# Optimization experiments

Measured on AMD Instinct MI355X. Metric: run time of the kernel, lower is better.

Reference implementation:

```python
import jax, jax.numpy as jnp
import numpy as np

N, IN, OUT, RANK = 8192, 4096, 4096, 16
SCALING = 2.0

def setup_inputs() -> dict:
    key = jax.random.key(0)
    k1, k2, k3, k4 = jax.random.split(key, 4)
    x = jax.random.normal(k1, (N, IN), dtype=jnp.float32)
    weight = jax.random.normal(k2, (OUT, IN), dtype=jnp.float32) * (1.0 / np.sqrt(IN))
    lora_A = jax.random.normal(k3, (RANK, IN), dtype=jnp.float32) * (1.0 / np.sqrt(IN))
    lora_B = jax.random.normal(k4, (OUT, RANK), dtype=jnp.float32) * 0.01
    return {"x": x, "weight": weight, "lora_A": lora_A, "lora_B": lora_B}

def reference(x, weight, lora_A, lora_B):
    # frozen base linear: F.linear(x, weight) == x @ weight.T  -> [N, OUT]
    base = jnp.einsum('ni,oi->no', x, weight)
    # LoRA branch: dropout(x) (p=0 => identity) @ A.T @ B.T, scaled
    lora = jnp.einsum('ni,ri->nr', x, lora_A)      # [N, RANK]
    lora = jnp.einsum('nr,or->no', lora, lora_B)   # [N, OUT]
    return base + lora * SCALING
```

## Files before the change

kernel.cpp:

```cpp
#include <hip/hip_runtime.h>


#define N_ROWS 8192
#define K_DIM  4096
#define N_COLS 4096
#define RANK   16
#define BK     32
#define NT     (K_DIM / BK)

#define XBLK ((N_ROWS * K_DIM / 4) / 256)
#define WBLK ((N_COLS * K_DIM / 4) / 256)

typedef __bf16 bf16x8 __attribute__((ext_vector_type(8)));
typedef float  f32x4  __attribute__((ext_vector_type(4)));

__device__ __forceinline__ unsigned short f2bf(float f) {
  unsigned int u = __builtin_bit_cast(unsigned int, f);
  u += 0x7FFFu + ((u >> 16) & 1u);
  return (unsigned short)(u >> 16);
}


__global__ __launch_bounds__(256) void prep_kernel(const float* __restrict__ x,
                                                   const float* __restrict__ w,
                                                   const float* __restrict__ A,
                                                   const float* __restrict__ Bm,
                                                   unsigned short* __restrict__ xb,
                                                   unsigned short* __restrict__ wb) {
  const int b = blockIdx.x;
  if (b < XBLK) {
    size_t idx = (size_t)b * 256 + threadIdx.x;
    const float4 v = *reinterpret_cast<const float4*>(x + idx * 4);
    ushort4 r;
    r.x = f2bf(v.x); r.y = f2bf(v.y); r.z = f2bf(v.z); r.w = f2bf(v.w);
    *reinterpret_cast<ushort4*>(xb + idx * 4) = r;
  } else {
    size_t idx = (size_t)(b - XBLK) * 256 + threadIdx.x;
    int o  = (int)(idx >> 10);
    int ic = (int)(idx & 1023) << 2;
    const float4 wv = *reinterpret_cast<const float4*>(w + (size_t)o * K_DIM + ic);
    float a0 = wv.x, a1 = wv.y, a2 = wv.z, a3 = wv.w;
    float br[RANK];
#pragma unroll
    for (int r4 = 0; r4 < RANK / 4; ++r4) {
      const float4 bv = *reinterpret_cast<const float4*>(Bm + (size_t)o * RANK + r4 * 4);
      br[r4 * 4 + 0] = bv.x; br[r4 * 4 + 1] = bv.y;
      br[r4 * 4 + 2] = bv.z; br[r4 * 4 + 3] = bv.w;
    }
#pragma unroll
    for (int r = 0; r < RANK; ++r) {
      const float4 av = *reinterpret_cast<const float4*>(A + (size_t)r * K_DIM + ic);
      float b2 = br[r] * 2.0f;
      a0 += b2 * av.x; a1 += b2 * av.y; a2 += b2 * av.z; a3 += b2 * av.w;
    }
    ushort4 rr;
    rr.x = f2bf(a0); rr.y = f2bf(a1); rr.z = f2bf(a2); rr.w = f2bf(a3);
    *reinterpret_cast<ushort4*>(wb + (size_t)o * K_DIM + ic) = rr;
  }
}


__device__ __forceinline__ void gload_lds16(const void* g, void* l) {
  __builtin_amdgcn_global_load_lds(
      (__attribute__((address_space(1))) void*)g,
      (__attribute__((address_space(3))) void*)l, 16, 0, 0);
}

__global__ __launch_bounds__(512, 1) void gemm_bf16_r10(
    const unsigned short* __restrict__ xb, const unsigned short* __restrict__ wb,
    float* __restrict__ out) {
  __shared__ __align__(16) char smem[131072];

  const int t  = threadIdx.x;
  const int l  = t & 63;
  const int wv = t >> 6;
  const int lr = l & 15;
  const int lk = l >> 4;
  const int wr = wv >> 2;
  const int wc = wv & 3;

  const int bid  = blockIdx.x;
  const int sbid = (bid & 7) * 64 + (bid >> 3);
  const int bm   = sbid >> 4;
  const int bn   = sbid & 15;

  const int slog  = (t & 7) ^ ((t >> 3) & 7);
  const int s_row = 2 * (t >> 3) + (slog >> 2);
  const int s_k   = (slog & 3) * 8;
  const unsigned short* gA = xb + (size_t)(bm * 256 + s_row) * K_DIM + s_k;
  const unsigned short* gB = wb + (size_t)(bn * 256 + s_row) * K_DIM + s_k;

#define STG_A(BUFB, KT) do {                                                    \
    const unsigned short* _g = gA + (size_t)(KT) * BK;                          \
    char* _l = smem + (BUFB) + t * 16;                                          \
    gload_lds16(_g, _l);                                                        \
    gload_lds16(_g + (size_t)128 * K_DIM, _l + 8192);                           \
  } while (0)
#define STG_B(BUFB, KT) do {                                                    \
    const unsigned short* _g = gB + (size_t)(KT) * BK;                          \
    char* _l = smem + (BUFB) + 16384 + t * 16;                                  \
    gload_lds16(_g, _l);                                                        \
    gload_lds16(_g + (size_t)128 * K_DIM, _l + 8192);                           \
  } while (0)

  const int lane_off = (lr >> 1) * 128 + (((((lr & 1) << 2) | lk) ^ (lr >> 1)) << 4);
  const int a_base = wr * 1024 + lane_off;
  const int b_base = 16384 + wc * 1024 + lane_off;

  bf16x8 sA0[8], sB0[4], sA1[8], sB1[4];
  f32x4 acc[8][4];
#pragma unroll
  for (int m = 0; m < 8; ++m)
#pragma unroll
    for (int n = 0; n < 4; ++n)
      acc[m][n] = (f32x4){0.f, 0.f, 0.f, 0.f};

#define RD_SET(SA, SB, RB) do {                                                 \
    _Pragma("unroll")                                                           \
    for (int m = 0; m < 8; ++m)                                                 \
      SA[m] = *(const bf16x8*)(smem + (RB) + a_base + m * 2048);                \
    _Pragma("unroll")                                                           \
    for (int n = 0; n < 4; ++n)                                                 \
      SB[n] = *(const bf16x8*)(smem + (RB) + b_base + n * 4096);                \
  } while (0)

#define MF_SET(SA, SB) do {                                                     \
    _Pragma("unroll")                                                           \
    for (int m = 0; m < 8; ++m)                                                 \
      _Pragma("unroll")                                                         \
      for (int n = 0; n < 4; ++n)                                               \
        acc[m][n] = __builtin_amdgcn_mfma_f32_16x16x32_bf16(                    \
            SA[m], SB[n], acc[m][n], 0, 0, 0);                                  \
  } while (0)

#define BODY(RB_OFF, SB_OFF, CUR_A, CUR_B, NXT_A, NXT_B, TT) do {               \
    const int _ts = ((TT) + 3 < NT) ? (TT) + 3 : NT - 1;                        \
    STG_A(SB_OFF, _ts); STG_B(SB_OFF, _ts);                                     \
    RD_SET(NXT_A, NXT_B, RB_OFF);                                               \
    __builtin_amdgcn_s_setprio(1);                                              \
    MF_SET(CUR_A, CUR_B);                                                       \
    __builtin_amdgcn_s_setprio(0);                                              \
    __builtin_amdgcn_sched_barrier(0);                                          \
    asm volatile("s_waitcnt vmcnt(4)");                                         \
    __builtin_amdgcn_s_barrier();                                               \
    __builtin_amdgcn_sched_barrier(0);                                          \
  } while (0)

  STG_A(0, 0);      STG_B(0, 0);
  STG_A(32768, 1);  STG_B(32768, 1);
  STG_A(65536, 2);  STG_B(65536, 2);
  __builtin_amdgcn_sched_barrier(0);
  asm volatile("s_waitcnt vmcnt(4)");
  __builtin_amdgcn_s_barrier();
  __builtin_amdgcn_sched_barrier(0);
  RD_SET(sA0, sB0, 0);

#pragma nounroll
  for (int u = 0; u < NT / 4; ++u) {
    const int tb = 4 * u;
    BODY(32768, 98304, sA0, sB0, sA1, sB1, tb);
    BODY(65536, 0,     sA1, sB1, sA0, sB0, tb + 1);
    BODY(98304, 32768, sA0, sB0, sA1, sB1, tb + 2);
    BODY(0,     65536, sA1, sB1, sA0, sB0, tb + 3);
  }

  const int orow = bm * 256 + wr * 16 + lk * 4;
  const int ocol = bn * 256 + wc * 16 + lr;
#pragma unroll
  for (int mf = 0; mf < 8; ++mf)
#pragma unroll
    for (int nf = 0; nf < 4; ++nf)
#pragma unroll
      for (int j = 0; j < 4; ++j)
        out[(size_t)(orow + mf * 32 + j) * N_COLS + (ocol + nf * 64)] = acc[mf][nf][j];

#undef STG_A
#undef STG_B
#undef RD_SET
#undef MF_SET
#undef BODY
}


__global__ __launch_bounds__(256) void fallback_kernel(const float* __restrict__ x,
                                                       const float* __restrict__ w,
                                                       const float* __restrict__ A,
                                                       const float* __restrict__ Bm,
                                                       float* __restrict__ out) {
  const int o    = blockIdx.x * 256 + threadIdx.x;
  const int nrow = blockIdx.y;
  float bro[RANK];
#pragma unroll
  for (int r = 0; r < RANK; ++r) bro[r] = Bm[(size_t)o * RANK + r] * 2.0f;
  float bacc = 0.f;
  float tacc[RANK];
#pragma unroll
  for (int r = 0; r < RANK; ++r) tacc[r] = 0.f;
  for (int k = 0; k < K_DIM; ++k) {
    float xv = x[(size_t)nrow * K_DIM + k];
    bacc += xv * w[(size_t)o * K_DIM + k];
#pragma unroll
    for (int r = 0; r < RANK; ++r) tacc[r] += xv * A[(size_t)r * K_DIM + k];
  }
  float res = bacc;
#pragma unroll
  for (int r = 0; r < RANK; ++r) res += bro[r] * tacc[r];
  out[(size_t)nrow * N_COLS + o] = res;
}


extern "C" void kernel_launch(void* const* d_in, const int* in_sizes, int n_in,
                              void* d_out, int out_size, void* d_ws, size_t ws_size,
                              hipStream_t stream) {
  const float* x  = (const float*)d_in[0];
  const float* w  = (const float*)d_in[1];
  const float* A  = (const float*)d_in[2];
  const float* Bm = (const float*)d_in[3];
  float* out = (float*)d_out;

  const size_t need = ((size_t)N_ROWS * K_DIM + (size_t)N_COLS * K_DIM) * sizeof(unsigned short);
  if (ws_size < need) {
    dim3 grid(N_COLS / 256, N_ROWS);
    fallback_kernel<<<grid, 256, 0, stream>>>(x, w, A, Bm, out);
    return;
  }

  unsigned short* xb = (unsigned short*)d_ws;
  unsigned short* wb = xb + (size_t)N_ROWS * K_DIM;

  prep_kernel<<<XBLK + WBLK, 256, 0, stream>>>(x, w, A, Bm, xb, wb);

  const int grid_gemm = (N_ROWS / 256) * (N_COLS / 256);
  gemm_bf16_r10<<<grid_gemm, 512, 0, stream>>>(xb, wb, out);
}
```

Baseline: 325.3 us.

## Shrink GEMM tile to 256x128 with double-buffered LDS for multi-block occupancy

The bf16 MFMA GEMM goes from a 256x256 tile with a 4-stage, 128KB LDS ring and a register-double-buffered fragment pipeline to a 256x128 tile with 48KB double-buffered LDS. Launch bounds now allow up to 4 blocks per CU, and the grid doubles. The aim is to hide latency through occupancy rather than deep software prefetch. In exchange, each step waits on vmcnt(0) with only one tile of lookahead, operand reuse per block is lower, and there is more global traffic for A.

```diff
diff --git a/kernel.cpp b/kernel.cpp
--- a/kernel.cpp
+++ b/kernel.cpp
@@ -5,8 +5,8 @@
 #define K_DIM  4096
 #define N_COLS 4096
 #define RANK   16
-#define BK     32
-#define NT     (K_DIM / BK)
+#define BKS    32
+#define NSTEP  (K_DIM / BKS)
 
 #define XBLK ((N_ROWS * K_DIM / 4) / 256)
 #define WBLK ((N_COLS * K_DIM / 4) / 256)
@@ -66,119 +66,109 @@
       (__attribute__((address_space(3))) void*)l, 16, 0, 0);
 }
 
-__global__ __launch_bounds__(512, 1) void gemm_bf16_r10(
+__global__ __launch_bounds__(512, 4) void gemm_bf16_r12(
     const unsigned short* __restrict__ xb, const unsigned short* __restrict__ wb,
     float* __restrict__ out) {
-  __shared__ __align__(16) char smem[131072];
+  __shared__ __align__(16) char smem[49152];
 
   const int t  = threadIdx.x;
   const int l  = t & 63;
   const int wv = t >> 6;
   const int lr = l & 15;
   const int lk = l >> 4;
-  const int wr = wv >> 2;
-  const int wc = wv & 3;
+  const int wr = wv >> 1;
+  const int wc = wv & 1;
 
   const int bid  = blockIdx.x;
-  const int sbid = (bid & 7) * 64 + (bid >> 3);
-  const int bm   = sbid >> 4;
-  const int bn   = sbid & 15;
+  const int sbid = (bid & 7) * 128 + (bid >> 3);
+  const int bm   = sbid >> 5;
+  const int bn   = sbid & 31;
 
   const int slog  = (t & 7) ^ ((t >> 3) & 7);
   const int s_row = 2 * (t >> 3) + (slog >> 2);
   const int s_k   = (slog & 3) * 8;
   const unsigned short* gA = xb + (size_t)(bm * 256 + s_row) * K_DIM + s_k;
-  const unsigned short* gB = wb + (size_t)(bn * 256 + s_row) * K_DIM + s_k;
-
-#define STG_A(BUFB, KT) do {                                                    \
-    const unsigned short* _g = gA + (size_t)(KT) * BK;                          \
-    char* _l = smem + (BUFB) + t * 16;                                          \
-    gload_lds16(_g, _l);                                                        \
-    gload_lds16(_g + (size_t)128 * K_DIM, _l + 8192);                           \
-  } while (0)
-#define STG_B(BUFB, KT) do {                                                    \
-    const unsigned short* _g = gB + (size_t)(KT) * BK;                          \
-    char* _l = smem + (BUFB) + 16384 + t * 16;                                  \
-    gload_lds16(_g, _l);                                                        \
-    gload_lds16(_g + (size_t)128 * K_DIM, _l + 8192);                           \
+  const unsigned short* gB = wb + (size_t)(bn * 128 + s_row) * K_DIM + s_k;
+  char* ldsA = smem + t * 16;
+  char* ldsB = smem + 16384 + t * 16;
+
+#define STG(BUFB, KT) do {                                                      \
+    const unsigned short* _ga = gA + (size_t)(KT) * BKS;                        \
+    const unsigned short* _gb = gB + (size_t)(KT) * BKS;                        \
+    gload_lds16(_ga, ldsA + (BUFB));                                            \
+    gload_lds16(_ga + (size_t)128 * K_DIM, ldsA + (BUFB) + 8192);               \
+    gload_lds16(_gb, ldsB + (BUFB));                                            \
   } while (0)
 
   const int lane_off = (lr >> 1) * 128 + (((((lr & 1) << 2) | lk) ^ (lr >> 1)) << 4);
-  const int a_base = wr * 1024 + lane_off;
-  const int b_base = 16384 + wc * 1024 + lane_off;
-
-  bf16x8 sA0[8], sB0[4], sA1[8], sB1[4];
-  f32x4 acc[8][4];
-#pragma unroll
-  for (int m = 0; m < 8; ++m)
+  const int a_base = wr * 4096 + lane_off;
+  const int b_base = 16384 + wc * 4096 + lane_off;
+
+  bf16x8 aF[4], bF[4];
+  f32x4 acc[4][4];
+#pragma unroll
+  for (int m = 0; m < 4; ++m)
 #pragma unroll
     for (int n = 0; n < 4; ++n)
       acc[m][n] = (f32x4){0.f, 0.f, 0.f, 0.f};
 
-#define RD_SET(SA, SB, RB) do {                                                 \
+#define RD(BUFB) do {                                                           \
     _Pragma("unroll")                                                           \
-    for (int m = 0; m < 8; ++m)                                                 \
-      SA[m] = *(const bf16x8*)(smem + (RB) + a_base + m * 2048);                \
+    for (int m = 0; m < 4; ++m)                                                 \
+      aF[m] = *(const bf16x8*)(smem + (BUFB) + a_base + m * 1024);              \
     _Pragma("unroll")                                                           \
     for (int n = 0; n < 4; ++n)                                                 \
-      SB[n] = *(const bf16x8*)(smem + (RB) + b_base + n * 4096);                \
-  } while (0)
-
-#define MF_SET(SA, SB) do {                                                     \
+      bF[n] = *(const bf16x8*)(smem + (BUFB) + b_base + n * 1024);              \
+  } while (0)
+
+#define MF() do {                                                               \
     _Pragma("unroll")                                                           \
-    for (int m = 0; m < 8; ++m)                                                 \
+    for (int m = 0; m < 4; ++m)                                                 \
       _Pragma("unroll")                                                         \
       for (int n = 0; n < 4; ++n)                                               \
         acc[m][n] = __builtin_amdgcn_mfma_f32_16x16x32_bf16(                    \
-            SA[m], SB[n], acc[m][n], 0, 0, 0);                                  \
-  } while (0)
-
-#define BODY(RB_OFF, SB_OFF, CUR_A, CUR_B, NXT_A, NXT_B, TT) do {               \
-    const int _ts = ((TT) + 3 < NT) ? (TT) + 3 : NT - 1;                        \
-    STG_A(SB_OFF, _ts); STG_B(SB_OFF, _ts);                                     \
-    RD_SET(NXT_A, NXT_B, RB_OFF);                                               \
+            aF[m], bF[n], acc[m][n], 0, 0, 0);                                  \
+  } while (0)
+
+#define STEP(CB, NB, T) do {                                                    \
+    const int _t1 = ((T) + 1 < NSTEP) ? (T) + 1 : NSTEP - 1;                    \
+    STG(NB, _t1);                                                               \
+    RD(CB);                                                                     \
     __builtin_amdgcn_s_setprio(1);                                              \
-    MF_SET(CUR_A, CUR_B);                                                       \
+    MF();                                                                       \
     __builtin_amdgcn_s_setprio(0);                                              \
     __builtin_amdgcn_sched_barrier(0);                                          \
-    asm volatile("s_waitcnt vmcnt(4)");                                         \
+    asm volatile("s_waitcnt vmcnt(0)");                                         \
     __builtin_amdgcn_s_barrier();                                               \
     __builtin_amdgcn_sched_barrier(0);                                          \
   } while (0)
 
-  STG_A(0, 0);      STG_B(0, 0);
-  STG_A(32768, 1);  STG_B(32768, 1);
-  STG_A(65536, 2);  STG_B(65536, 2);
+  STG(0, 0);
   __builtin_amdgcn_sched_barrier(0);
-  asm volatile("s_waitcnt vmcnt(4)");
+  asm volatile("s_waitcnt vmcnt(0)");
   __builtin_amdgcn_s_barrier();
   __builtin_amdgcn_sched_barrier(0);
-  RD_SET(sA0, sB0, 0);
 
 #pragma nounroll
-  for (int u = 0; u < NT / 4; ++u) {
-    const int tb = 4 * u;
-    BODY(32768, 98304, sA0, sB0, sA1, sB1, tb);
-    BODY(65536, 0,     sA1, sB1, sA0, sB0, tb + 1);
-    BODY(98304, 32768, sA0, sB0, sA1, sB1, tb + 2);
-    BODY(0,     65536, sA1, sB1, sA0, sB0, tb + 3);
-  }
-
-  const int orow = bm * 256 + wr * 16 + lk * 4;
-  const int ocol = bn * 256 + wc * 16 + lr;
-#pragma unroll
-  for (int mf = 0; mf < 8; ++mf)
+  for (int u = 0; u < NSTEP / 2; ++u) {
+    STEP(0, 24576, 2 * u);
+    STEP(24576, 0, 2 * u + 1);
+  }
+
+  const int orow = bm * 256 + wr * 64 + lk * 4;
+  const int ocol = bn * 128 + wc * 64 + lr;
+#pragma unroll
+  for (int mf = 0; mf < 4; ++mf)
 #pragma unroll
     for (int nf = 0; nf < 4; ++nf)
 #pragma unroll
       for (int j = 0; j < 4; ++j)
-        out[(size_t)(orow + mf * 32 + j) * N_COLS + (ocol + nf * 64)] = acc[mf][nf][j];
-
-#undef STG_A
-#undef STG_B
-#undef RD_SET
-#undef MF_SET
-#undef BODY
+        out[(size_t)(orow + mf * 16 + j) * N_COLS + (ocol + nf * 16)] = acc[mf][nf][j];
+
+#undef STG
+#undef RD
+#undef MF
+#undef STEP
 }
 
 
@@ -230,6 +220,6 @@
 
   prep_kernel<<<XBLK + WBLK, 256, 0, stream>>>(x, w, A, Bm, xb, wb);
 
-  const int grid_gemm = (N_ROWS / 256) * (N_COLS / 256);
-  gemm_bf16_r10<<<grid_gemm, 512, 0, stream>>>(xb, wb, out);
-}
+  const int grid_gemm = (N_ROWS / 256) * (N_COLS / 128);
+  gemm_bf16_r12<<<grid_gemm, 512, 0, stream>>>(xb, wb, out);
+}
```

Result: slower. 353.2 us (+8.6%).
